# Kernel tuning notes

Hardware: AMD Instinct MI355X
Metric: run time of the kernel (lower is better)

## Reference

```python
import jax, jax.numpy as jnp
import numpy as np

T = 500_000  # sequence length
K = 16       # number of hidden states


def setup_inputs() -> dict:
    key = jax.random.key(0)
    k1, k2, k3, k4 = jax.random.split(key, 4)
    y = jax.random.normal(k1, (T,), dtype=jnp.float32)
    transition_logits = jax.random.normal(k2, (K, K), dtype=jnp.float32)
    mu = 2.0 * jax.random.normal(k3, (K,), dtype=jnp.float32)
    log_sigma = 0.1 * jax.random.normal(k4, (K,), dtype=jnp.float32)
    return {"y": y, "transition_logits": transition_logits, "mu": mu, "log_sigma": log_sigma}


def _stationary_distribution(P):
    # Solve pi P = pi, sum(pi) = 1 via least squares (normal equations: differentiable, jit-safe).
    k = P.shape[0]
    A = jnp.concatenate([P.T - jnp.eye(k, dtype=P.dtype), jnp.ones((1, k), dtype=P.dtype)], axis=0)
    b = jnp.concatenate([jnp.zeros((k,), dtype=P.dtype), jnp.ones((1,), dtype=P.dtype)])
    return jnp.linalg.solve(A.T @ A, A.T @ b)


def reference(y, transition_logits, mu, log_sigma):
    P = jax.nn.softmax(transition_logits, axis=-1)  # [K, K] row-stochastic transition matrix
    sigma = jnp.exp(log_sigma)
    # Gaussian emission densities g[t, k] = N(y_t; mu_k, sigma_k^2)
    z = (y[:, None] - mu[None, :]) / sigma[None, :]
    INV_SQRT_2PI = 0.3989422804014327
    g = jnp.exp(-0.5 * z * z) * (INV_SQRT_2PI / sigma)[None, :]  # [T, K]

    ut0 = _stationary_distribution(P)              # [K]
    g0 = g[0]
    ft0 = jnp.sum(ut0 * g0)                        # scalar
    utt0 = ut0 * g0 / ft0                          # [K]

    def step(utt_prev, gt):
        ut = utt_prev @ P                          # predictive dist [K]
        ft = jnp.sum(ut * gt)                      # normalizer
        utt = ut * gt / ft                         # filtered posterior [K]
        return utt, (ut, ft, utt)

    _, (Ut, ft_rest, Utt) = jax.lax.scan(step, utt0, g[1:])

    ut = jnp.concatenate([ut0[None, :], Ut], axis=0)       # [T, K]
    u_norm = jnp.concatenate([utt0[None, :], Utt], axis=0)  # [T, K]
    ft = jnp.concatenate([ft0[None], ft_rest], axis=0)      # [T]
    return (ut, u_norm, ft)
```

## Files before the change

### kernel.cpp

```cpp
#include <hip/hip_runtime.h>

#define CHUNK_L 32
#define WARMUP_W 16

typedef _Float16 h16;
typedef _Float16 h16x4 __attribute__((ext_vector_type(4)));
typedef float f32x4 __attribute__((ext_vector_type(4)));

static __device__ __forceinline__ f32x4 mfma16(h16x4 a, h16x4 b, f32x4 c) {
#if __has_builtin(__builtin_amdgcn_mfma_f32_16x16x16f16)
    return __builtin_amdgcn_mfma_f32_16x16x16f16(a, b, c, 0, 0, 0);
#else
    f32x4 d;
    asm volatile("v_mfma_f32_16x16x16_f16 %0, %1, %2, %3\n\ts_nop 7\n\ts_nop 7"
                 : "=v"(d) : "v"(a), "v"(b), "v"(c));
    return d;
#endif
}

__global__ __launch_bounds__(256, 4) void hmm_filter_kernel(
    const float* __restrict__ y,
    const float* __restrict__ logits,
    const float* __restrict__ mu,
    const float* __restrict__ log_sigma,
    float* __restrict__ out,
    int T, int nchunks)
{
    __shared__ float Plds[256];
    __shared__ float Ba[256];
    __shared__ float Bb[256];

    const int tid = (int)threadIdx.x;
    const int j   = tid & 15;
    const int gr  = tid >> 4;

    float l = logits[tid];
    float m = l;
    #pragma unroll
    for (int s = 1; s < 16; s <<= 1) m = fmaxf(m, __shfl_xor(m, s, 16));
    float e = __expf(l - m);
    float rs = e;
    #pragma unroll
    for (int s = 1; s < 16; s <<= 1) rs += __shfl_xor(rs, s, 16);
    float Pv = e / rs;
    Plds[tid] = Pv;
    Ba[tid]   = Pv;
    __syncthreads();

    float* cur = Ba;
    float* nxt = Bb;
    for (int itq = 0; itq < 10; ++itq) {
        float acc = 0.f;
        #pragma unroll
        for (int k = 0; k < 16; ++k)
            acc += cur[gr * 16 + k] * cur[k * 16 + j];
        float rsum = acc;
        #pragma unroll
        for (int s = 1; s < 16; s <<= 1) rsum += __shfl_xor(rsum, s, 16);
        nxt[tid] = acc / rsum;
        __syncthreads();
        float* tmp = cur; cur = nxt; nxt = tmp;
    }

    const int lane = tid & 63;
    const int col  = lane & 15;
    const int i0   = (lane >> 4) << 2;
    const int wv   = ((int)blockIdx.x << 2) + (tid >> 6);
    const int cbase = wv << 4;

    h16x4 Ahi, Alo;
    #pragma unroll
    for (int ee = 0; ee < 4; ++ee) {
        float a = Plds[(i0 + ee) * 16 + col];
        h16 hi = (h16)a;
        Ahi[ee] = hi;
        Alo[ee] = (h16)(a - (float)hi);
    }

    h16x4 bhi, blo;
    #pragma unroll
    for (int ee = 0; ee < 4; ++ee) {
        float pv = cur[i0 + ee];
        h16 hi = (h16)pv;
        bhi[ee] = hi;
        blo[ee] = (h16)(pv - (float)hi);
    }

    float isv[4], nmv[4], lcv[4];
    #pragma unroll
    for (int ee = 0; ee < 4; ++ee) {
        int st = i0 + ee;
        float is = __expf(-log_sigma[st]);
        isv[ee] = is;
        nmv[ee] = -mu[st] * is;
        lcv[ee] = __log2f(0.3989422804014327f * is);
    }
    const float K2 = -0.7213475204444817f;

    if (cbase >= nchunks) return;

    const int chunk = cbase + col;
    const bool live = chunk < nchunks;
    const bool isC0 = (chunk == 0);
    const int Tm4 = T - 4;
    const int TN  = T << 4;

    int tb = chunk * CHUNK_L - WARMUP_W;

    auto yld = [&](int t) -> float4 {
        int tc = t < 0 ? 0 : (t > Tm4 ? Tm4 : t);
        return *(const float4*)(y + tc);
    };

    float4 c4 = yld(tb);
    float4 n1 = yld(tb + 4);

    float r1 = 1.0f;

#define FSTEP(YT, WARM, DOST, UTP, UNP, FDST)  do {                       \
    f32x4 D = {0.f, 0.f, 0.f, 0.f};                                       \
    D = mfma16(Ahi, bhi, D);                                              \
    D = mfma16(Alo, bhi, D);                                              \
    D = mfma16(Ahi, blo, D);                                              \
    f32x4 eg;                                                             \
    _Pragma("unroll")                                                     \
    for (int ee = 0; ee < 4; ++ee) {                                      \
        float z  = fmaf((YT), isv[ee], nmv[ee]);                          \
        float gg = __builtin_amdgcn_exp2f(fmaf(z * z, K2, lcv[ee]));      \
        if (WARM) gg = isC0 ? 1.0f : gg;                                  \
        eg[ee] = gg * r1;                                                 \
    }                                                                     \
    f32x4 pg = D * eg;                                                    \
    float sv = (pg.x + pg.y) + (pg.z + pg.w);                             \
    sv += __shfl_xor(sv, 16);                                             \
    sv += __shfl_xor(sv, 32);                                             \
    float rv = __builtin_amdgcn_rcpf(sv);                                 \
    if ((DOST) && live) {                                                 \
        f32x4 ut = D * r1;                                                \
        f32x4 un = pg * rv;                                               \
        *(f32x4*)(UTP) = ut;                                              \
        *(f32x4*)(UNP) = un;                                              \
    }                                                                     \
    if (DOST) { FDST = sv; }                                              \
    _Pragma("unroll")                                                     \
    for (int ee = 0; ee < 4; ++ee) {                                      \
        h16 hh = (h16)pg[ee];                                             \
        bhi[ee] = hh;                                                     \
        blo[ee] = (h16)(pg[ee] - (float)hh);                              \
    }                                                                     \
    r1 = rv;                                                              \
} while (0)

    float fdummy;
    #pragma unroll 1
    for (int b = 0; b < WARMUP_W / 4; ++b) {
        float4 nn = yld(tb + 8);
        FSTEP(c4.x, true, false, out, out, fdummy);
        FSTEP(c4.y, true, false, out, out, fdummy);
        FSTEP(c4.z, true, false, out, out, fdummy);
        FSTEP(c4.w, true, false, out, out, fdummy);
        c4 = n1; n1 = nn; tb += 4;
    }
    (void)fdummy;

    float* pU = out + ((chunk * CHUNK_L) << 4) + i0;
    float* pN = pU + TN;
    float* pF = out + 2 * TN + chunk * CHUNK_L;
    f32x4 f4;

    #pragma unroll 1
    for (int b = 0; b < CHUNK_L / 4; ++b) {
        float4 nn = yld(tb + 8);
        FSTEP(c4.x, false, true, pU,      pN,      f4.x);
        FSTEP(c4.y, false, true, pU + 16, pN + 16, f4.y);
        FSTEP(c4.z, false, true, pU + 32, pN + 32, f4.z);
        FSTEP(c4.w, false, true, pU + 48, pN + 48, f4.w);
        if (lane < 16 && live) *(f32x4*)(pF) = f4;
        pU += 64; pN += 64; pF += 4;
        c4 = n1; n1 = nn; tb += 4;
    }
#undef FSTEP
}

extern "C" void kernel_launch(void* const* d_in, const int* in_sizes, int n_in,
                              void* d_out, int out_size, void* d_ws, size_t ws_size,
                              hipStream_t stream) {
    const float* y      = (const float*)d_in[0];
    const float* logits = (const float*)d_in[1];
    const float* mu     = (const float*)d_in[2];
    const float* ls     = (const float*)d_in[3];
    float* out = (float*)d_out;
    const int T = in_sizes[0];

    const int nchunks = (T + CHUNK_L - 1) / CHUNK_L;
    const int nwaves  = (nchunks + 15) / 16;
    const int blocks  = (nwaves + 3) / 4;
    hmm_filter_kernel<<<blocks, 256, 0, stream>>>(y, logits, mu, ls, out,
                                                  T, nchunks);
}
```

Before: 89.64 us.

## Stage filter outputs in LDS per wave for coalesced global stores

```diff
diff --git a/kernel.cpp b/kernel.cpp
--- a/kernel.cpp
+++ b/kernel.cpp
@@ -18,7 +18,7 @@
 #endif
 }
 
-__global__ __launch_bounds__(256, 4) void hmm_filter_kernel(
+__global__ __launch_bounds__(256, 2) void hmm_filter_kernel(
     const float* __restrict__ y,
     const float* __restrict__ logits,
     const float* __restrict__ mu,
@@ -29,6 +29,7 @@
     __shared__ float Plds[256];
     __shared__ float Ba[256];
     __shared__ float Bb[256];
+    __shared__ float SD[4 * 2048 + 4 * 512];
 
     const int tid = (int)threadIdx.x;
     const int j   = tid & 15;
@@ -64,14 +65,17 @@
 
     const int lane = tid & 63;
     const int col  = lane & 15;
-    const int i0   = (lane >> 4) << 2;
+    const int g4   = (lane >> 4) << 2;
     const int wv   = ((int)blockIdx.x << 2) + (tid >> 6);
     const int cbase = wv << 4;
 
+    const int wbase = (tid >> 6) * 2048;
+    const int ftb   = 8192 + (tid >> 6) * 512;
+
     h16x4 Ahi, Alo;
     #pragma unroll
     for (int ee = 0; ee < 4; ++ee) {
-        float a = Plds[(i0 + ee) * 16 + col];
+        float a = Plds[(g4 + ee) * 16 + col];
         h16 hi = (h16)a;
         Ahi[ee] = hi;
         Alo[ee] = (h16)(a - (float)hi);
@@ -80,7 +84,7 @@
     h16x4 bhi, blo;
     #pragma unroll
     for (int ee = 0; ee < 4; ++ee) {
-        float pv = cur[i0 + ee];
+        float pv = cur[g4 + ee];
         h16 hi = (h16)pv;
         bhi[ee] = hi;
         blo[ee] = (h16)(pv - (float)hi);
@@ -89,7 +93,7 @@
     float isv[4], nmv[4], lcv[4];
     #pragma unroll
     for (int ee = 0; ee < 4; ++ee) {
-        int st = i0 + ee;
+        int st = g4 + ee;
         float is = __expf(-log_sigma[st]);
         isv[ee] = is;
         nmv[ee] = -mu[st] * is;
@@ -100,7 +104,6 @@
     if (cbase >= nchunks) return;
 
     const int chunk = cbase + col;
-    const bool live = chunk < nchunks;
     const bool isC0 = (chunk == 0);
     const int Tm4 = T - 4;
     const int TN  = T << 4;
@@ -117,7 +120,7 @@
 
     float r1 = 1.0f;
 
-#define FSTEP(YT, WARM, DOST, UTP, UNP, FDST)  do {                       \
+#define FSTEPW(YT)  do {                                                  \
     f32x4 D = {0.f, 0.f, 0.f, 0.f};                                       \
     D = mfma16(Ahi, bhi, D);                                              \
     D = mfma16(Alo, bhi, D);                                              \
@@ -127,21 +130,13 @@
     for (int ee = 0; ee < 4; ++ee) {                                      \
         float z  = fmaf((YT), isv[ee], nmv[ee]);                          \
         float gg = __builtin_amdgcn_exp2f(fmaf(z * z, K2, lcv[ee]));      \
-        if (WARM) gg = isC0 ? 1.0f : gg;                                  \
-        eg[ee] = gg * r1;                                                 \
+        eg[ee] = (isC0 ? 1.0f : gg) * r1;                                 \
     }                                                                     \
     f32x4 pg = D * eg;                                                    \
     float sv = (pg.x + pg.y) + (pg.z + pg.w);                             \
     sv += __shfl_xor(sv, 16);                                             \
     sv += __shfl_xor(sv, 32);                                             \
     float rv = __builtin_amdgcn_rcpf(sv);                                 \
-    if ((DOST) && live) {                                                 \
-        f32x4 ut = D * r1;                                                \
-        f32x4 un = pg * rv;                                               \
-        *(f32x4*)(UTP) = ut;                                              \
-        *(f32x4*)(UNP) = un;                                              \
-    }                                                                     \
-    if (DOST) { FDST = sv; }                                              \
     _Pragma("unroll")                                                     \
     for (int ee = 0; ee < 4; ++ee) {                                      \
         h16 hh = (h16)pg[ee];                                             \
@@ -151,35 +146,82 @@
     r1 = rv;                                                              \
 } while (0)
 
-    float fdummy;
+#define FSTEPS(YT, TS, FDST)  do {                                        \
+    f32x4 D = {0.f, 0.f, 0.f, 0.f};                                       \
+    D = mfma16(Ahi, bhi, D);                                              \
+    D = mfma16(Alo, bhi, D);                                              \
+    D = mfma16(Ahi, blo, D);                                              \
+    f32x4 eg;                                                             \
+    _Pragma("unroll")                                                     \
+    for (int ee = 0; ee < 4; ++ee) {                                      \
+        float z  = fmaf((YT), isv[ee], nmv[ee]);                          \
+        float gg = __builtin_amdgcn_exp2f(fmaf(z * z, K2, lcv[ee]));      \
+        eg[ee] = gg * r1;                                                 \
+    }                                                                     \
+    f32x4 pg = D * eg;                                                    \
+    float sv = (pg.x + pg.y) + (pg.z + pg.w);                             \
+    sv += __shfl_xor(sv, 16);                                             \
+    sv += __shfl_xor(sv, 32);                                             \
+    float rv = __builtin_amdgcn_rcpf(sv);                                 \
+    *(f32x4*)(SD + wbase + col * 64 + (TS) * 16 + g4)        = D * r1;    \
+    *(f32x4*)(SD + wbase + col * 64 + (TS) * 16 + g4 + 1024) = pg * rv;   \
+    FDST = sv;                                                            \
+    _Pragma("unroll")                                                     \
+    for (int ee = 0; ee < 4; ++ee) {                                      \
+        h16 hh = (h16)pg[ee];                                             \
+        bhi[ee] = hh;                                                     \
+        blo[ee] = (h16)(pg[ee] - (float)hh);                              \
+    }                                                                     \
+    r1 = rv;                                                              \
+} while (0)
+
     #pragma unroll 1
     for (int b = 0; b < WARMUP_W / 4; ++b) {
         float4 nn = yld(tb + 8);
-        FSTEP(c4.x, true, false, out, out, fdummy);
-        FSTEP(c4.y, true, false, out, out, fdummy);
-        FSTEP(c4.z, true, false, out, out, fdummy);
-        FSTEP(c4.w, true, false, out, out, fdummy);
+        FSTEPW(c4.x);
+        FSTEPW(c4.y);
+        FSTEPW(c4.z);
+        FSTEPW(c4.w);
         c4 = n1; n1 = nn; tb += 4;
     }
-    (void)fdummy;
-
-    float* pU = out + ((chunk * CHUNK_L) << 4) + i0;
-    float* pN = pU + TN;
-    float* pF = out + 2 * TN + chunk * CHUNK_L;
+
     f32x4 f4;
-
     #pragma unroll 1
     for (int b = 0; b < CHUNK_L / 4; ++b) {
         float4 nn = yld(tb + 8);
-        FSTEP(c4.x, false, true, pU,      pN,      f4.x);
-        FSTEP(c4.y, false, true, pU + 16, pN + 16, f4.y);
-        FSTEP(c4.z, false, true, pU + 32, pN + 32, f4.z);
-        FSTEP(c4.w, false, true, pU + 48, pN + 48, f4.w);
-        if (lane < 16 && live) *(f32x4*)(pF) = f4;
-        pU += 64; pN += 64; pF += 4;
+        FSTEPS(c4.x, 0, f4.x);
+        FSTEPS(c4.y, 1, f4.y);
+        FSTEPS(c4.z, 2, f4.z);
+        FSTEPS(c4.w, 3, f4.w);
+        if (lane < 16) *(f32x4*)(SD + ftb + col * 32 + b * 4) = f4;
+
+        #pragma unroll
+        for (int i = 0; i < 4; ++i) {
+            const int cc = cbase + i * 4 + (lane >> 4);
+            const int li = wbase + (i * 4 + (lane >> 4)) * 64 + (lane & 15) * 4;
+            f32x4 vu = *(f32x4*)(SD + li);
+            f32x4 vn = *(f32x4*)(SD + li + 1024);
+            if (cc < nchunks) {
+                float* dst = out + (size_t)cc * 512 + b * 64 + (lane & 15) * 4;
+                *(f32x4*)dst        = vu;
+                *(f32x4*)(dst + TN) = vn;
+            }
+        }
         c4 = n1; n1 = nn; tb += 4;
     }
-#undef FSTEP
+
+    {
+        const int cc0 = cbase + (lane >> 2);
+        if (cc0 < nchunks) {
+            f32x4 a  = *(f32x4*)(SD + ftb + lane * 8);
+            f32x4 bq = *(f32x4*)(SD + ftb + lane * 8 + 4);
+            float* dst = out + 2 * (size_t)TN + (size_t)cbase * 32 + lane * 8;
+            *(f32x4*)dst       = a;
+            *(f32x4*)(dst + 4) = bq;
+        }
+    }
+#undef FSTEPW
+#undef FSTEPS
 }
 
 extern "C" void kernel_launch(void* const* d_in, const int* in_sizes, int n_in,
```

Result: slower. 94.24 us (+5.1%).
